# Performance work log

Measured on AMD Instinct MI355X. Metric: run time of the kernel, lower is better.

The kernel has to match this reference:

```python
import jax, jax.numpy as jnp
import numpy as np

B, C_IN, C_MID, C_OUT, H, W = 256, 2, 128, 64, 15, 15
N_RES = 4  # line_length//2 - 1 with line_length=11

# per-direction input offsets for kernel taps w0 and w2 (w1 is always center),
# matching fix_direction_order=True sparse 3x3 kernel construction:
# dir0 horizontal, dir1 vertical, dir2 anti-diagonal, dir3 main diagonal.
OFFSETS = (((0, -1), (0, 1)),
           ((-1, 0), (1, 0)),
           ((1, -1), (-1, 1)),
           ((-1, -1), (1, 1)))


def shift2d(x, di, dj):
    # out[..., i, j] = x[..., i+di, j+dj] with zero padding (di,dj in {-1,0,1})
    nd = x.ndim
    xp = jnp.pad(x, [(0, 0)] * (nd - 2) + [(1, 1), (1, 1)])
    h, w = x.shape[-2], x.shape[-1]
    return xp[..., 1 + di:1 + di + h, 1 + dj:1 + dj + w]


def dir_conv(x, w, b):
    # x: [4,B,Cin,H,W]; w: [Cout,Cin,3]; b: [Cout]
    x0 = jnp.stack([shift2d(x[d], *OFFSETS[d][0]) for d in range(4)])
    x2 = jnp.stack([shift2d(x[d], *OFFSETS[d][1]) for d in range(4)])
    y = (jnp.einsum('oc,dbchw->dbohw', w[..., 0], x0)
         + jnp.einsum('oc,dbchw->dbohw', w[..., 1], x)
         + jnp.einsum('oc,dbchw->dbohw', w[..., 2], x2))
    return y + b[None, None, :, None, None]


def conv1x1(x, w, b):
    # x: [4,B,Cin,H,W]; w: [Cout,Cin]; b: [Cout]
    return jnp.einsum('oc,dbchw->dbohw', w, x) + b[None, None, :, None, None]


def setup_inputs() -> dict:
    key = jax.random.key(0)
    ks = jax.random.split(key, 16)
    s_in = 1.0 / np.sqrt(3 * C_IN)
    s_mid = 1.0 / np.sqrt(3 * C_MID)
    s_pw = 1.0 / np.sqrt(C_MID)
    return {
        'x': jax.random.normal(ks[0], (B, C_IN, H, W), jnp.float32),
        'dconv0_w': jax.random.normal(ks[1], (C_MID, C_IN, 3), jnp.float32) * s_in,
        'dconv0_b': jnp.zeros((C_MID,), jnp.float32),
        'res_dconv_w': jax.random.normal(ks[2], (N_RES, C_MID, C_MID, 3), jnp.float32) * s_mid,
        'res_dconv_b': jnp.zeros((N_RES, C_MID), jnp.float32),
        'res_pw_w': jax.random.normal(ks[3], (N_RES, C_MID, C_MID), jnp.float32) * s_pw,
        'res_pw_b': jnp.zeros((N_RES, C_MID), jnp.float32),
        'c0_w1': jax.random.normal(ks[4], (C_MID, C_MID), jnp.float32) * s_pw,
        'c0_b1': jnp.zeros((C_MID,), jnp.float32),
        'c0_w2': jax.random.normal(ks[5], (C_MID, C_MID), jnp.float32) * s_pw,
        'c0_b2': jnp.zeros((C_MID,), jnp.float32),
        'final_w': jax.random.normal(ks[6], (C_OUT, C_MID), jnp.float32) * s_pw,
        'final_b': jnp.zeros((C_OUT,), jnp.float32),
    }


def reference(x, dconv0_w, dconv0_b, res_dconv_w, res_dconv_b,
              res_pw_w, res_pw_b, c0_w1, c0_b1, c0_w2, c0_b2,
              final_w, final_b):
    act = jax.nn.silu
    # all 4 direction streams start from the same input plane
    h = jnp.broadcast_to(x[None], (4,) + x.shape)  # [4,B,Cin,H,W]
    h = act(dir_conv(h, dconv0_w, dconv0_b))
    # DirectionalConvResBlocks (norm='none')
    for i in range(N_RES):
        r = h
        h = act(dir_conv(h, res_dconv_w[i], res_dconv_b[i]))
        h = act(conv1x1(h, res_pw_w[i], res_pw_b[i]))
        h = h + r
    # Conv0dResBlock (two 1x1 convs, middle_dim_multipler=1)
    r = h
    h = act(conv1x1(h, c0_w1, c0_b1))
    h = act(conv1x1(h, c0_w2, c0_b2))
    h = h + r
    # final 1x1 conv, then stack directions at dim=1 -> [B,4,Cout,H,W]
    h = conv1x1(h, final_w, final_b)
    return jnp.transpose(h, (1, 0, 2, 3, 4))
```

## Files before the change

kernel.cpp:

```cpp
#include <hip/hip_runtime.h>

using u16 = unsigned short;
using u32 = unsigned int;

typedef __bf16 bf16x8 __attribute__((ext_vector_type(8)));
typedef float  f32x4  __attribute__((ext_vector_type(4)));

#define NPOS   225
#define NT     15
#define ROWP   136
#define A_ROWS 289
#define B_ROWS 241
#define A_ELEMS (A_ROWS*ROWP)
#define B_ELEMS (B_ROWS*ROWP)
#define LDS_BYTES ((A_ELEMS + B_ELEMS)*2)
#define RSTRIDE17 (17*ROWP)

#define WA_PER_L 49152
#define WP_OFF   (4*WA_PER_L)
#define WP_PER   16384
#define WF_OFF   (WP_OFF + 6*WP_PER)
#define W_U16_TOTAL (WF_OFF + 8192)

__device__ __forceinline__ float bflo(u32 q){ return __uint_as_float(q << 16); }
__device__ __forceinline__ float bfhi(u32 q){ return __uint_as_float(q & 0xffff0000u); }
__device__ __forceinline__ u16 f2bf(float f){
  u32 u = __float_as_uint(f);
  return (u16)((u + 0x7fffu + ((u >> 16) & 1u)) >> 16);
}
__device__ __forceinline__ u32 packbf(float a, float b){
  union { __bf16 h[2]; u32 u; } r;
  r.h[0] = (__bf16)a; r.h[1] = (__bf16)b;
  return r.u;
}
__device__ __forceinline__ float silu_f(float x){
  return x * __builtin_amdgcn_rcpf(1.f + __expf(-x));
}
__device__ __forceinline__ f32x4 mfma16(bf16x8 a, bf16x8 b, f32x4 c){
  return __builtin_amdgcn_mfma_f32_16x16x32_bf16(a, b, c, 0, 0, 0);
}

__global__ void prep_w(const float* __restrict__ d0w, const float* __restrict__ rdw,
                       const float* __restrict__ rpw, const float* __restrict__ c1w,
                       const float* __restrict__ c2w, const float* __restrict__ fw,
                       float* __restrict__ ws)
{
  u16* wsb = (u16*)(ws + 768);
  const int total = 768 + W_U16_TOTAL;
  for (int idx = blockIdx.x*blockDim.x + threadIdx.x; idx < total; idx += gridDim.x*blockDim.x){
    if (idx < 768){
      int k = idx >> 7, o = idx & 127;
      ws[idx] = d0w[o*6 + k];
      continue;
    }
    int e = idx - 768;
    float v;
    if (e < WP_OFF){
      int L = e / WA_PER_L, r = e % WA_PER_L;
      int w = r / 6144, r2 = r % 6144;
      int t = r2 >> 11, r3 = r2 & 2047;
      int kb = r3 >> 9, r4 = r3 & 511;
      int l = r4 >> 3, j = r4 & 7;
      int o = w*16 + (l & 15);
      int c = kb*32 + ((l >> 4) << 3) + j;
      v = rdw[((L*128 + o)*128 + c)*3 + t];
    } else if (e < WF_OFF){
      int t2 = e - WP_OFF;
      int i = t2 / WP_PER, r = t2 % WP_PER;
      int w = r >> 11, r2 = r & 2047;
      int kb = r2 >> 9, r3 = r2 & 511;
      int l = r3 >> 3, j = r3 & 7;
      int o = w*16 + (l & 15);
      int c = kb*32 + ((l >> 4) << 3) + j;
      v = (i < 4) ? rpw[(i*128 + o)*128 + c]
        : (i == 4) ? c1w[o*128 + c] : c2w[o*128 + c];
    } else {
      int e2 = e - WF_OFF;
      int ot = e2 >> 11, r = e2 & 2047;
      int kb = r >> 9, r2 = r & 511;
      int l = r2 >> 3, j = r2 & 7;
      int o = ot*16 + (l & 15);
      int c = kb*32 + ((l >> 4) << 3) + j;
      v = fw[o*128 + c];
    }
    wsb[e] = f2bf(v);
  }
}

__device__ __forceinline__ void dconv_mfma(const u16* __restrict__ As, u16* __restrict__ Bs,
    const u16* __restrict__ wloc, const float* __restrict__ bias,
    int lane, int og, int T0, int T1, int off0, int off2)
{
  const int col = lane & 15, kg = lane >> 4, koff = kg*8;
  bf16x8 wa[2][12];
  #pragma unroll
  for (int ot=0; ot<2; ++ot)
    #pragma unroll
    for (int f=0; f<12; ++f)
      wa[ot][f] = *(const bf16x8*)(wloc + (2*og+ot)*6144 + f*512 + lane*8);
  f32x4 bz0 = *(const f32x4*)(bias + (2*og)*16 + kg*4);
  f32x4 bz1 = *(const f32x4*)(bias + (2*og+1)*16 + kg*4);
  const int c1 = (col+1)*ROWP;
  #pragma unroll 1
  for (int tile=T0; tile<T1; ++tile){
    int rb = (tile+1)*RSTRIDE17 + c1;
    const u16* s0 = As + rb + off0 + koff;
    const u16* s1 = As + rb + koff;
    const u16* s2 = As + rb + off2 + koff;
    f32x4 a0 = bz0, a1 = bz1;
    #pragma unroll
    for (int kb=0; kb<4; ++kb){
      bf16x8 v0 = *(const bf16x8*)(s0 + kb*32);
      bf16x8 v1 = *(const bf16x8*)(s1 + kb*32);
      bf16x8 v2 = *(const bf16x8*)(s2 + kb*32);
      a0 = mfma16(wa[0][kb],   v0, a0); a1 = mfma16(wa[1][kb],   v0, a1);
      a0 = mfma16(wa[0][4+kb], v1, a0); a1 = mfma16(wa[1][4+kb], v1, a1);
      a0 = mfma16(wa[0][8+kb], v2, a0); a1 = mfma16(wa[1][8+kb], v2, a1);
    }
    if (col < 15){
      u16* dp = Bs + (tile*16+col)*ROWP + og*32 + kg*4;
      uint2 w0; w0.x = packbf(silu_f(a0[0]), silu_f(a0[1]));
      w0.y = packbf(silu_f(a0[2]), silu_f(a0[3]));
      *(uint2*)dp = w0;
      uint2 w1; w1.x = packbf(silu_f(a1[0]), silu_f(a1[1]));
      w1.y = packbf(silu_f(a1[2]), silu_f(a1[3]));
      *(uint2*)(dp+16) = w1;
    }
  }
}

template<bool SRC_HALO, bool DST_HALO, bool RESID>
__device__ __forceinline__ void pw_mfma(const u16* __restrict__ src, u16* __restrict__ dst,
    const u16* __restrict__ wloc, const float* __restrict__ bias,
    int lane, int og, int T0, int T1)
{
  const int col = lane & 15, kg = lane >> 4, koff = kg*8;
  bf16x8 wp[2][4];
  #pragma unroll
  for (int ot=0; ot<2; ++ot)
    #pragma unroll
    for (int kb=0; kb<4; ++kb)
      wp[ot][kb] = *(const bf16x8*)(wloc + (2*og+ot)*2048 + kb*512 + lane*8);
  f32x4 bz0 = *(const f32x4*)(bias + (2*og)*16 + kg*4);
  f32x4 bz1 = *(const f32x4*)(bias + (2*og+1)*16 + kg*4);
  const int c1 = (col+1)*ROWP;
  #pragma unroll 1
  for (int tile=T0; tile<T1; ++tile){
    int rsrc = SRC_HALO ? (tile+1)*RSTRIDE17 + c1 : (tile*16+col)*ROWP;
    int rdst = DST_HALO ? (tile+1)*RSTRIDE17 + c1 : (tile*16+col)*ROWP;
    const u16* s = src + rsrc + koff;
    f32x4 a0 = bz0, a1 = bz1;
    #pragma unroll
    for (int kb=0; kb<4; ++kb){
      bf16x8 v = *(const bf16x8*)(s + kb*32);
      a0 = mfma16(wp[0][kb], v, a0);
      a1 = mfma16(wp[1][kb], v, a1);
    }
    if (col < 15){
      u16* dp = dst + rdst + og*32 + kg*4;
      float s0 = silu_f(a0[0]), s1 = silu_f(a0[1]), s2 = silu_f(a0[2]), s3 = silu_f(a0[3]);
      float t0 = silu_f(a1[0]), t1 = silu_f(a1[1]), t2 = silu_f(a1[2]), t3 = silu_f(a1[3]);
      if (RESID){
        uint2 r0 = *(const uint2*)dp;
        uint2 r1 = *(const uint2*)(dp+16);
        s0 += bflo(r0.x); s1 += bfhi(r0.x); s2 += bflo(r0.y); s3 += bfhi(r0.y);
        t0 += bflo(r1.x); t1 += bfhi(r1.x); t2 += bflo(r1.y); t3 += bfhi(r1.y);
      }
      uint2 w0; w0.x = packbf(s0, s1); w0.y = packbf(s2, s3);
      *(uint2*)dp = w0;
      uint2 w1; w1.x = packbf(t0, t1); w1.y = packbf(t2, t3);
      *(uint2*)(dp+16) = w1;
    }
  }
}

__global__ void __launch_bounds__(512, 2)
mix9_main(const float* __restrict__ x,
          const float* __restrict__ b_d0,
          const float* __restrict__ b_rd,
          const float* __restrict__ b_rp,
          const float* __restrict__ b_c1,
          const float* __restrict__ b_c2,
          const float* __restrict__ b_fin,
          const float* __restrict__ wt,
          float* __restrict__ out)
{
  extern __shared__ u16 sm[];
  u16* As = sm;
  u16* Bs = sm + A_ELEMS;

  const int blk  = blockIdx.x;
  const int b    = blk >> 2, d = blk & 3;
  const int tid  = threadIdx.x;
  const int wave = __builtin_amdgcn_readfirstlane(tid >> 6);
  const int lane = tid & 63;
  const int og   = wave >> 1;
  const int ph   = wave & 1;
  const int T0   = ph * 8;
  const int T1   = ph ? NT : 8;
  const int ob   = wave * 16;

  const int DI0[4] = {0,-1, 1,-1}, DJ0[4] = {-1, 0,-1,-1};
  const int DI2[4] = {0, 1,-1, 1}, DJ2[4] = { 1, 0, 1, 1};
  const int di0 = DI0[d], dj0 = DJ0[d], di2 = DI2[d], dj2 = DJ2[d];
  const int off0 = (di0*17 + dj0)*ROWP;
  const int off2 = (di2*17 + dj2)*ROWP;

  for (int k2 = tid; k2 < A_ELEMS; k2 += 512) As[k2] = 0;
  float* xs = (float*)Bs;
  for (int k2 = tid; k2 < 2*NPOS; k2 += 512) xs[k2] = x[b*(2*NPOS) + k2];
  __syncthreads();

  #pragma unroll 1
  for (int pb = 0; pb < 4; ++pb){
    int pp = pb*64 + lane;
    int i = pp >> 4, j = pp & 15;
    if (i >= 15 || j >= 15) continue;
    float acc[16];
    #pragma unroll
    for (int oo=0;oo<16;++oo) acc[oo] = b_d0[ob+oo];
    #pragma unroll
    for (int c=0;c<2;++c){
      int i0=i+di0, j0=j+dj0, i2=i+di2, j2=j+dj2;
      float x0 = ((unsigned)i0<15u && (unsigned)j0<15u) ? xs[c*NPOS + i0*15 + j0] : 0.f;
      float x1 = xs[c*NPOS + i*15 + j];
      float x2 = ((unsigned)i2<15u && (unsigned)j2<15u) ? xs[c*NPOS + i2*15 + j2] : 0.f;
      const float* w0r = wt + (c*3+0)*128 + ob;
      const float* w1r = wt + (c*3+1)*128 + ob;
      const float* w2r = wt + (c*3+2)*128 + ob;
      #pragma unroll
      for (int oo=0;oo<16;++oo)
        acc[oo] = fmaf(w0r[oo],x0, fmaf(w1r[oo],x1, fmaf(w2r[oo],x2, acc[oo])));
    }
    u16* dp = As + ((i+1)*17 + (j+1))*ROWP + ob;
    #pragma unroll
    for (int oo=0;oo<16;oo+=2)
      *(u32*)(dp+oo) = packbf(silu_f(acc[oo]), silu_f(acc[oo+1]));
  }
  __syncthreads();

  const u16* wsb = (const u16*)(wt + 768);

  #pragma unroll 1
  for (int L = 0; L < 4; ++L){
    dconv_mfma(As, Bs, wsb + L*WA_PER_L, b_rd + L*128, lane, og, T0, T1, off0, off2);
    __syncthreads();
    pw_mfma<false,true,true>(Bs, As, wsb + WP_OFF + L*WP_PER, b_rp + L*128, lane, og, T0, T1);
    __syncthreads();
  }

  pw_mfma<true,false,false>(As, Bs, wsb + WP_OFF + 4*WP_PER, b_c1, lane, og, T0, T1);
  __syncthreads();
  pw_mfma<false,true,true>(Bs, As, wsb + WP_OFF + 5*WP_PER, b_c2, lane, og, T0, T1);
  __syncthreads();

  {
    const int col = lane & 15, kg = lane >> 4, koff = kg*8;
    const u16* wl = wsb + WF_OFF + og*2048;
    bf16x8 wf[4];
    #pragma unroll
    for (int kb=0;kb<4;++kb) wf[kb] = *(const bf16x8*)(wl + (kb*64 + lane)*8);
    f32x4 bias4 = *(const f32x4*)(b_fin + og*16 + kg*4);
    const int c1 = (col+1)*ROWP;
    #pragma unroll 1
    for (int tile = T0; tile < T1; ++tile){
      int rb = (tile+1)*RSTRIDE17 + c1;
      const u16* s = As + rb + koff;
      f32x4 acc = bias4;
      #pragma unroll
      for (int kb=0;kb<4;++kb)
        acc = mfma16(wf[kb], *(const bf16x8*)(s + kb*32), acc);
      if (col < 15){
        float* op = out + ((size_t)((b*4 + d)*64 + og*16 + kg*4))*NPOS + tile*15 + col;
        op[0]      = acc[0];
        op[NPOS]   = acc[1];
        op[2*NPOS] = acc[2];
        op[3*NPOS] = acc[3];
      }
    }
  }
}

extern "C" void kernel_launch(void* const* d_in, const int* in_sizes, int n_in,
                              void* d_out, int out_size, void* d_ws, size_t ws_size,
                              hipStream_t stream)
{
  const float* x     = (const float*)d_in[0];
  const float* w_d0  = (const float*)d_in[1];
  const float* b_d0  = (const float*)d_in[2];
  const float* w_rd  = (const float*)d_in[3];
  const float* b_rd  = (const float*)d_in[4];
  const float* w_rp  = (const float*)d_in[5];
  const float* b_rp  = (const float*)d_in[6];
  const float* w_c1  = (const float*)d_in[7];
  const float* b_c1  = (const float*)d_in[8];
  const float* w_c2  = (const float*)d_in[9];
  const float* b_c2  = (const float*)d_in[10];
  const float* w_fin = (const float*)d_in[11];
  const float* b_fin = (const float*)d_in[12];
  float* wt  = (float*)d_ws;
  float* out = (float*)d_out;

  prep_w<<<128, 512, 0, stream>>>(w_d0, w_rd, w_rp, w_c1, w_c2, w_fin, wt);

  (void)hipFuncSetAttribute((const void*)mix9_main,
                            hipFuncAttributeMaxDynamicSharedMemorySize, LDS_BYTES);
  mix9_main<<<1024, 512, LDS_BYTES, stream>>>(x, b_d0, b_rd, b_rp, b_c1, b_c2, b_fin, wt, out);
}
```

Baseline: 239.8 us.

## Swizzle LDS activation rows with XOR instead of padding; widen pointwise tiles

Replaces the padded 136-element LDS row stride with an unpadded 128-element stride and an XOR swizzle on the channel offset keyed by row index, intended to avoid bank conflicts while shrinking LDS footprint. The pointwise convs now assign 4 output tiles per wave over a quarter of the spatial tiles instead of 2 tiles over half, reusing each loaded activation vector across more MFMAs. It also adds s_setprio around MFMA blocks and unrolls the pointwise loop by 2. Risks include higher register pressure from 16 weight fragments and swizzle index math overhead.

New measurement: 257.3 us. 1.07x slower.

```diff
diff --git a/kernel.cpp b/kernel.cpp
--- a/kernel.cpp
+++ b/kernel.cpp
@@ -8,13 +8,11 @@
 
 #define NPOS   225
 #define NT     15
-#define ROWP   136
 #define A_ROWS 289
-#define B_ROWS 241
-#define A_ELEMS (A_ROWS*ROWP)
-#define B_ELEMS (B_ROWS*ROWP)
+#define B_ROWS 240
+#define A_ELEMS (A_ROWS*128)
+#define B_ELEMS (B_ROWS*128)
 #define LDS_BYTES ((A_ELEMS + B_ELEMS)*2)
-#define RSTRIDE17 (17*ROWP)
 
 #define WA_PER_L 49152
 #define WP_OFF   (4*WA_PER_L)
@@ -89,9 +87,10 @@
 
 __device__ __forceinline__ void dconv_mfma(const u16* __restrict__ As, u16* __restrict__ Bs,
     const u16* __restrict__ wloc, const float* __restrict__ bias,
-    int lane, int og, int T0, int T1, int off0, int off2)
-{
-  const int col = lane & 15, kg = lane >> 4, koff = kg*8;
+    int lane, int og, int T0, int T1, int dr0, int dr2)
+{
+  const int col = lane & 15, kg = lane >> 4;
+  const int k0 = kg*8;
   bf16x8 wa[2][12];
   #pragma unroll
   for (int ot=0; ot<2; ++ot)
@@ -100,77 +99,95 @@
       wa[ot][f] = *(const bf16x8*)(wloc + (2*og+ot)*6144 + f*512 + lane*8);
   f32x4 bz0 = *(const f32x4*)(bias + (2*og)*16 + kg*4);
   f32x4 bz1 = *(const f32x4*)(bias + (2*og+1)*16 + kg*4);
-  const int c1 = (col+1)*ROWP;
+  const int chb = og*32 + kg*4;
+  int r1 = (T0+1)*17 + col + 1;
+  int p2 = T0*16 + col;
   #pragma unroll 1
   for (int tile=T0; tile<T1; ++tile){
-    int rb = (tile+1)*RSTRIDE17 + c1;
-    const u16* s0 = As + rb + off0 + koff;
-    const u16* s1 = As + rb + koff;
-    const u16* s2 = As + rb + off2 + koff;
+    int ra = r1 + dr0, rc = r1 + dr2;
+    int sa = (ra&15)<<3, sb = (r1&15)<<3, sc = (rc&15)<<3;
+    const u16* A0 = As + (ra<<7);
+    const u16* A1 = As + (r1<<7);
+    const u16* A2 = As + (rc<<7);
     f32x4 a0 = bz0, a1 = bz1;
+    __builtin_amdgcn_s_setprio(1);
     #pragma unroll
     for (int kb=0; kb<4; ++kb){
-      bf16x8 v0 = *(const bf16x8*)(s0 + kb*32);
-      bf16x8 v1 = *(const bf16x8*)(s1 + kb*32);
-      bf16x8 v2 = *(const bf16x8*)(s2 + kb*32);
+      const int kk = k0 + kb*32;
+      bf16x8 v0 = *(const bf16x8*)(A0 + (kk ^ sa));
+      bf16x8 v1 = *(const bf16x8*)(A1 + (kk ^ sb));
+      bf16x8 v2 = *(const bf16x8*)(A2 + (kk ^ sc));
       a0 = mfma16(wa[0][kb],   v0, a0); a1 = mfma16(wa[1][kb],   v0, a1);
       a0 = mfma16(wa[0][4+kb], v1, a0); a1 = mfma16(wa[1][4+kb], v1, a1);
       a0 = mfma16(wa[0][8+kb], v2, a0); a1 = mfma16(wa[1][8+kb], v2, a1);
     }
+    __builtin_amdgcn_s_setprio(0);
     if (col < 15){
-      u16* dp = Bs + (tile*16+col)*ROWP + og*32 + kg*4;
+      int idx = (p2<<7) + (chb ^ ((p2&15)<<3));
       uint2 w0; w0.x = packbf(silu_f(a0[0]), silu_f(a0[1]));
       w0.y = packbf(silu_f(a0[2]), silu_f(a0[3]));
-      *(uint2*)dp = w0;
+      *(uint2*)(Bs + idx) = w0;
       uint2 w1; w1.x = packbf(silu_f(a1[0]), silu_f(a1[1]));
       w1.y = packbf(silu_f(a1[2]), silu_f(a1[3]));
-      *(uint2*)(dp+16) = w1;
-    }
+      *(uint2*)(Bs + (idx ^ 16)) = w1;
+    }
+    r1 += 17; p2 += 16;
   }
 }
 
 template<bool SRC_HALO, bool DST_HALO, bool RESID>
 __device__ __forceinline__ void pw_mfma(const u16* __restrict__ src, u16* __restrict__ dst,
     const u16* __restrict__ wloc, const float* __restrict__ bias,
-    int lane, int og, int T0, int T1)
-{
-  const int col = lane & 15, kg = lane >> 4, koff = kg*8;
-  bf16x8 wp[2][4];
+    int lane, int og2, int T0, int T1)
+{
+  const int col = lane & 15, kg = lane >> 4;
+  const int k0 = kg*8;
+  bf16x8 wp[4][4];
   #pragma unroll
-  for (int ot=0; ot<2; ++ot)
+  for (int ot=0; ot<4; ++ot)
     #pragma unroll
     for (int kb=0; kb<4; ++kb)
-      wp[ot][kb] = *(const bf16x8*)(wloc + (2*og+ot)*2048 + kb*512 + lane*8);
-  f32x4 bz0 = *(const f32x4*)(bias + (2*og)*16 + kg*4);
-  f32x4 bz1 = *(const f32x4*)(bias + (2*og+1)*16 + kg*4);
-  const int c1 = (col+1)*ROWP;
-  #pragma unroll 1
+      wp[ot][kb] = *(const bf16x8*)(wloc + (og2*4+ot)*2048 + kb*512 + lane*8);
+  f32x4 bz[4];
+  #pragma unroll
+  for (int ot=0; ot<4; ++ot) bz[ot] = *(const f32x4*)(bias + og2*64 + ot*16 + kg*4);
+  const int chb = og2*64 + kg*4;
+  int r1 = (T0+1)*17 + col + 1;
+  int p2 = T0*16 + col;
+  #pragma unroll 2
   for (int tile=T0; tile<T1; ++tile){
-    int rsrc = SRC_HALO ? (tile+1)*RSTRIDE17 + c1 : (tile*16+col)*ROWP;
-    int rdst = DST_HALO ? (tile+1)*RSTRIDE17 + c1 : (tile*16+col)*ROWP;
-    const u16* s = src + rsrc + koff;
-    f32x4 a0 = bz0, a1 = bz1;
+    int rs = SRC_HALO ? r1 : p2;
+    const u16* S = src + (rs<<7);
+    int ss = (rs&15)<<3;
+    f32x4 a0 = bz[0], a1 = bz[1], a2 = bz[2], a3 = bz[3];
+    __builtin_amdgcn_s_setprio(1);
     #pragma unroll
     for (int kb=0; kb<4; ++kb){
-      bf16x8 v = *(const bf16x8*)(s + kb*32);
+      bf16x8 v = *(const bf16x8*)(S + ((k0 + kb*32) ^ ss));
       a0 = mfma16(wp[0][kb], v, a0);
       a1 = mfma16(wp[1][kb], v, a1);
-    }
+      a2 = mfma16(wp[2][kb], v, a2);
+      a3 = mfma16(wp[3][kb], v, a3);
+    }
+    __builtin_amdgcn_s_setprio(0);
     if (col < 15){
-      u16* dp = dst + rdst + og*32 + kg*4;
-      float s0 = silu_f(a0[0]), s1 = silu_f(a0[1]), s2 = silu_f(a0[2]), s3 = silu_f(a0[3]);
-      float t0 = silu_f(a1[0]), t1 = silu_f(a1[1]), t2 = silu_f(a1[2]), t3 = silu_f(a1[3]);
-      if (RESID){
-        uint2 r0 = *(const uint2*)dp;
-        uint2 r1 = *(const uint2*)(dp+16);
-        s0 += bflo(r0.x); s1 += bfhi(r0.x); s2 += bflo(r0.y); s3 += bfhi(r0.y);
-        t0 += bflo(r1.x); t1 += bfhi(r1.x); t2 += bflo(r1.y); t3 += bfhi(r1.y);
+      int rd = DST_HALO ? r1 : p2;
+      int idx0 = (rd<<7) + (chb ^ ((rd&15)<<3));
+      f32x4 aa[4] = {a0, a1, a2, a3};
+      #pragma unroll
+      for (int ot=0; ot<4; ++ot){
+        int idx = idx0 ^ (ot<<4);
+        float s0 = silu_f(aa[ot][0]), s1 = silu_f(aa[ot][1]);
+        float s2 = silu_f(aa[ot][2]), s3 = silu_f(aa[ot][3]);
+        if (RESID){
+          uint2 r = *(const uint2*)(dst + idx);
+          s0 += bflo(r.x); s1 += bfhi(r.x); s2 += bflo(r.y); s3 += bfhi(r.y);
+        }
+        uint2 w0; w0.x = packbf(s0, s1); w0.y = packbf(s2, s3);
+        *(uint2*)(dst + idx) = w0;
       }
-      uint2 w0; w0.x = packbf(s0, s1); w0.y = packbf(s2, s3);
-      *(uint2*)dp = w0;
-      uint2 w1; w1.x = packbf(t0, t1); w1.y = packbf(t2, t3);
-      *(uint2*)(dp+16) = w1;
-    }
+    }
+    r1 += 17; p2 += 16;
   }
 }
 
@@ -198,13 +215,17 @@
   const int ph   = wave & 1;
   const int T0   = ph * 8;
   const int T1   = ph ? NT : 8;
+  const int og2  = wave >> 2;
+  const int ph4  = wave & 3;
+  const int T0p  = ph4 * 4;
+  const int T1p  = (ph4 == 3) ? NT : T0p + 4;
   const int ob   = wave * 16;
 
   const int DI0[4] = {0,-1, 1,-1}, DJ0[4] = {-1, 0,-1,-1};
   const int DI2[4] = {0, 1,-1, 1}, DJ2[4] = { 1, 0, 1, 1};
   const int di0 = DI0[d], dj0 = DJ0[d], di2 = DI2[d], dj2 = DJ2[d];
-  const int off0 = (di0*17 + dj0)*ROWP;
-  const int off2 = (di2*17 + dj2)*ROWP;
+  const int dr0 = di0*17 + dj0;
+  const int dr2 = di2*17 + dj2;
 
   for (int k2 = tid; k2 < A_ELEMS; k2 += 512) As[k2] = 0;
   float* xs = (float*)Bs;
@@ -232,10 +253,12 @@
       for (int oo=0;oo<16;++oo)
         acc[oo] = fmaf(w0r[oo],x0, fmaf(w1r[oo],x1, fmaf(w2r[oo],x2, acc[oo])));
     }
-    u16* dp = As + ((i+1)*17 + (j+1))*ROWP + ob;
+    int r = (i+1)*17 + (j+1);
+    int s = (r&15)<<3;
+    u16* rowp = As + (r<<7);
     #pragma unroll
     for (int oo=0;oo<16;oo+=2)
-      *(u32*)(dp+oo) = packbf(silu_f(acc[oo]), silu_f(acc[oo+1]));
+      *(u32*)(rowp + ((ob+oo) ^ s)) = packbf(silu_f(acc[oo]), silu_f(acc[oo+1]));
   }
   __syncthreads();
 
@@ -243,33 +266,34 @@
 
   #pragma unroll 1
   for (int L = 0; L < 4; ++L){
-    dconv_mfma(As, Bs, wsb + L*WA_PER_L, b_rd + L*128, lane, og, T0, T1, off0, off2);
+    dconv_mfma(As, Bs, wsb + L*WA_PER_L, b_rd + L*128, lane, og, T0, T1, dr0, dr2);
     __syncthreads();
-    pw_mfma<false,true,true>(Bs, As, wsb + WP_OFF + L*WP_PER, b_rp + L*128, lane, og, T0, T1);
+    pw_mfma<false,true,true>(Bs, As, wsb + WP_OFF + L*WP_PER, b_rp + L*128, lane, og2, T0p, T1p);
     __syncthreads();
   }
 
-  pw_mfma<true,false,false>(As, Bs, wsb + WP_OFF + 4*WP_PER, b_c1, lane, og, T0, T1);
+  pw_mfma<true,false,false>(As, Bs, wsb + WP_OFF + 4*WP_PER, b_c1, lane, og2, T0p, T1p);
   __syncthreads();
-  pw_mfma<false,true,true>(Bs, As, wsb + WP_OFF + 5*WP_PER, b_c2, lane, og, T0, T1);
+  pw_mfma<false,true,true>(Bs, As, wsb + WP_OFF + 5*WP_PER, b_c2, lane, og2, T0p, T1p);
   __syncthreads();
 
   {
-    const int col = lane & 15, kg = lane >> 4, koff = kg*8;
+    const int col = lane & 15, kg = lane >> 4;
+    const int k0 = kg*8;
     const u16* wl = wsb + WF_OFF + og*2048;
     bf16x8 wf[4];
     #pragma unroll
     for (int kb=0;kb<4;++kb) wf[kb] = *(const bf16x8*)(wl + (kb*64 + lane)*8);
     f32x4 bias4 = *(const f32x4*)(b_fin + og*16 + kg*4);
-    const int c1 = (col+1)*ROWP;
+    int r1 = (T0+1)*17 + col + 1;
     #pragma unroll 1
     for (int tile = T0; tile < T1; ++tile){
-      int rb = (tile+1)*RSTRIDE17 + c1;
-      const u16* s = As + rb + koff;
+      const u16* S = As + (r1<<7);
+      int ss = (r1&15)<<3;
       f32x4 acc = bias4;
       #pragma unroll
       for (int kb=0;kb<4;++kb)
-        acc = mfma16(wf[kb], *(const bf16x8*)(s + kb*32), acc);
+        acc = mfma16(wf[kb], *(const bf16x8*)(S + ((k0 + kb*32) ^ ss)), acc);
       if (col < 15){
         float* op = out + ((size_t)((b*4 + d)*64 + og*16 + kg*4))*NPOS + tile*15 + col;
         op[0]      = acc[0];
@@ -277,6 +301,7 @@
         op[2*NPOS] = acc[2];
         op[3*NPOS] = acc[3];
       }
+      r1 += 17;
     }
   }
 }
```

## Double block to 1024 threads and repartition waves across output tiles and channels

Applied to the files above, without the earlier changes.

The block grows from 8 to 16 waves. The directional conv gives each wave a single 16-channel output tile instead of two. The pointwise layers split the 15 position tiles four ways across wave groups, and the first layer and final conv are redistributed to match. s_setprio is raised around the MFMA loops and the pointwise tile loop is unrolled by 2. More waves per block can better hide LDS latency, but launch_bounds(1024,1) and the LDS size allow only one block per CU where two were allowed before, and each wave now reuses fewer A-fragment loads.

Result: no change. 244.3 us (+1.9%).

```diff
diff --git a/kernel.cpp b/kernel.cpp
--- a/kernel.cpp
+++ b/kernel.cpp
@@ -89,17 +89,14 @@
 
 __device__ __forceinline__ void dconv_mfma(const u16* __restrict__ As, u16* __restrict__ Bs,
     const u16* __restrict__ wloc, const float* __restrict__ bias,
-    int lane, int og, int T0, int T1, int off0, int off2)
+    int lane, int ot, int T0, int T1, int off0, int off2)
 {
   const int col = lane & 15, kg = lane >> 4, koff = kg*8;
-  bf16x8 wa[2][12];
+  bf16x8 wa[12];
   #pragma unroll
-  for (int ot=0; ot<2; ++ot)
-    #pragma unroll
-    for (int f=0; f<12; ++f)
-      wa[ot][f] = *(const bf16x8*)(wloc + (2*og+ot)*6144 + f*512 + lane*8);
-  f32x4 bz0 = *(const f32x4*)(bias + (2*og)*16 + kg*4);
-  f32x4 bz1 = *(const f32x4*)(bias + (2*og+1)*16 + kg*4);
+  for (int f=0; f<12; ++f)
+    wa[f] = *(const bf16x8*)(wloc + ot*6144 + f*512 + lane*8);
+  f32x4 bz = *(const f32x4*)(bias + ot*16 + kg*4);
   const int c1 = (col+1)*ROWP;
   #pragma unroll 1
   for (int tile=T0; tile<T1; ++tile){
@@ -107,24 +104,23 @@
     const u16* s0 = As + rb + off0 + koff;
     const u16* s1 = As + rb + koff;
     const u16* s2 = As + rb + off2 + koff;
-    f32x4 a0 = bz0, a1 = bz1;
+    f32x4 a0 = bz;
+    __builtin_amdgcn_s_setprio(1);
     #pragma unroll
     for (int kb=0; kb<4; ++kb){
       bf16x8 v0 = *(const bf16x8*)(s0 + kb*32);
       bf16x8 v1 = *(const bf16x8*)(s1 + kb*32);
       bf16x8 v2 = *(const bf16x8*)(s2 + kb*32);
-      a0 = mfma16(wa[0][kb],   v0, a0); a1 = mfma16(wa[1][kb],   v0, a1);
-      a0 = mfma16(wa[0][4+kb], v1, a0); a1 = mfma16(wa[1][4+kb], v1, a1);
-      a0 = mfma16(wa[0][8+kb], v2, a0); a1 = mfma16(wa[1][8+kb], v2, a1);
-    }
+      a0 = mfma16(wa[kb],   v0, a0);
+      a0 = mfma16(wa[4+kb], v1, a0);
+      a0 = mfma16(wa[8+kb], v2, a0);
+    }
+    __builtin_amdgcn_s_setprio(0);
     if (col < 15){
-      u16* dp = Bs + (tile*16+col)*ROWP + og*32 + kg*4;
+      u16* dp = Bs + (tile*16+col)*ROWP + ot*16 + kg*4;
       uint2 w0; w0.x = packbf(silu_f(a0[0]), silu_f(a0[1]));
       w0.y = packbf(silu_f(a0[2]), silu_f(a0[3]));
       *(uint2*)dp = w0;
-      uint2 w1; w1.x = packbf(silu_f(a1[0]), silu_f(a1[1]));
-      w1.y = packbf(silu_f(a1[2]), silu_f(a1[3]));
-      *(uint2*)(dp+16) = w1;
     }
   }
 }
@@ -132,7 +128,7 @@
 template<bool SRC_HALO, bool DST_HALO, bool RESID>
 __device__ __forceinline__ void pw_mfma(const u16* __restrict__ src, u16* __restrict__ dst,
     const u16* __restrict__ wloc, const float* __restrict__ bias,
-    int lane, int og, int T0, int T1)
+    int lane, int og2, int T0, int T1)
 {
   const int col = lane & 15, kg = lane >> 4, koff = kg*8;
   bf16x8 wp[2][4];
@@ -140,31 +136,36 @@
   for (int ot=0; ot<2; ++ot)
     #pragma unroll
     for (int kb=0; kb<4; ++kb)
-      wp[ot][kb] = *(const bf16x8*)(wloc + (2*og+ot)*2048 + kb*512 + lane*8);
-  f32x4 bz0 = *(const f32x4*)(bias + (2*og)*16 + kg*4);
-  f32x4 bz1 = *(const f32x4*)(bias + (2*og+1)*16 + kg*4);
+      wp[ot][kb] = *(const bf16x8*)(wloc + (og2*2+ot)*2048 + kb*512 + lane*8);
+  f32x4 bz0 = *(const f32x4*)(bias + og2*32 + kg*4);
+  f32x4 bz1 = *(const f32x4*)(bias + og2*32 + 16 + kg*4);
+  const int chb = og2*32 + kg*4;
   const int c1 = (col+1)*ROWP;
-  #pragma unroll 1
+  #pragma unroll 2
   for (int tile=T0; tile<T1; ++tile){
-    int rsrc = SRC_HALO ? (tile+1)*RSTRIDE17 + c1 : (tile*16+col)*ROWP;
-    int rdst = DST_HALO ? (tile+1)*RSTRIDE17 + c1 : (tile*16+col)*ROWP;
-    const u16* s = src + rsrc + koff;
+    int r1 = (tile+1)*17 + col + 1;
+    int p2 = tile*16 + col;
+    int rsrc = SRC_HALO ? r1*ROWP : p2*ROWP;
+    const u16* S = src + rsrc + koff;
     f32x4 a0 = bz0, a1 = bz1;
+    __builtin_amdgcn_s_setprio(1);
     #pragma unroll
     for (int kb=0; kb<4; ++kb){
-      bf16x8 v = *(const bf16x8*)(s + kb*32);
+      bf16x8 v = *(const bf16x8*)(S + kb*32);
       a0 = mfma16(wp[0][kb], v, a0);
       a1 = mfma16(wp[1][kb], v, a1);
     }
+    __builtin_amdgcn_s_setprio(0);
     if (col < 15){
-      u16* dp = dst + rdst + og*32 + kg*4;
+      int rdst = DST_HALO ? r1*ROWP : p2*ROWP;
+      u16* dp = dst + rdst + chb;
       float s0 = silu_f(a0[0]), s1 = silu_f(a0[1]), s2 = silu_f(a0[2]), s3 = silu_f(a0[3]);
       float t0 = silu_f(a1[0]), t1 = silu_f(a1[1]), t2 = silu_f(a1[2]), t3 = silu_f(a1[3]);
       if (RESID){
         uint2 r0 = *(const uint2*)dp;
-        uint2 r1 = *(const uint2*)(dp+16);
+        uint2 r1v = *(const uint2*)(dp+16);
         s0 += bflo(r0.x); s1 += bfhi(r0.x); s2 += bflo(r0.y); s3 += bfhi(r0.y);
-        t0 += bflo(r1.x); t1 += bfhi(r1.x); t2 += bflo(r1.y); t3 += bfhi(r1.y);
+        t0 += bflo(r1v.x); t1 += bfhi(r1v.x); t2 += bflo(r1v.y); t3 += bfhi(r1v.y);
       }
       uint2 w0; w0.x = packbf(s0, s1); w0.y = packbf(s2, s3);
       *(uint2*)dp = w0;
@@ -174,7 +175,7 @@
   }
 }
 
-__global__ void __launch_bounds__(512, 2)
+__global__ void __launch_bounds__(1024, 1)
 mix9_main(const float* __restrict__ x,
           const float* __restrict__ b_d0,
           const float* __restrict__ b_rd,
@@ -194,11 +195,17 @@
   const int tid  = threadIdx.x;
   const int wave = __builtin_amdgcn_readfirstlane(tid >> 6);
   const int lane = tid & 63;
-  const int og   = wave >> 1;
-  const int ph   = wave & 1;
-  const int T0   = ph * 8;
-  const int T1   = ph ? NT : 8;
-  const int ob   = wave * 16;
+
+  const int ogd  = wave >> 1;
+  const int phd  = wave & 1;
+  const int T0d  = phd * 8;
+  const int T1d  = phd ? NT : 8;
+  const int og2  = wave >> 2;
+  const int ph4  = wave & 3;
+  const int T0p  = ph4 * 4;
+  const int T1p  = (ph4 == 3) ? NT : T0p + 4;
+  const int ob   = (wave & 7) * 16;
+  const int phal = wave >> 3;
 
   const int DI0[4] = {0,-1, 1,-1}, DJ0[4] = {-1, 0,-1,-1};
   const int DI2[4] = {0, 1,-1, 1}, DJ2[4] = { 1, 0, 1, 1};
@@ -206,14 +213,14 @@
   const int off0 = (di0*17 + dj0)*ROWP;
   const int off2 = (di2*17 + dj2)*ROWP;
 
-  for (int k2 = tid; k2 < A_ELEMS; k2 += 512) As[k2] = 0;
+  for (int k2 = tid; k2 < A_ELEMS; k2 += 1024) As[k2] = 0;
   float* xs = (float*)Bs;
-  for (int k2 = tid; k2 < 2*NPOS; k2 += 512) xs[k2] = x[b*(2*NPOS) + k2];
+  for (int k2 = tid; k2 < 2*NPOS; k2 += 1024) xs[k2] = x[b*(2*NPOS) + k2];
   __syncthreads();
 
   #pragma unroll 1
-  for (int pb = 0; pb < 4; ++pb){
-    int pp = pb*64 + lane;
+  for (int pb = 0; pb < 2; ++pb){
+    int pp = phal*128 + pb*64 + lane;
     int i = pp >> 4, j = pp & 15;
     if (i >= 15 || j >= 15) continue;
     float acc[16];
@@ -243,35 +250,39 @@
 
   #pragma unroll 1
   for (int L = 0; L < 4; ++L){
-    dconv_mfma(As, Bs, wsb + L*WA_PER_L, b_rd + L*128, lane, og, T0, T1, off0, off2);
+    dconv_mfma(As, Bs, wsb + L*WA_PER_L, b_rd + L*128, lane, ogd, T0d, T1d, off0, off2);
     __syncthreads();
-    pw_mfma<false,true,true>(Bs, As, wsb + WP_OFF + L*WP_PER, b_rp + L*128, lane, og, T0, T1);
+    pw_mfma<false,true,true>(Bs, As, wsb + WP_OFF + L*WP_PER, b_rp + L*128, lane, og2, T0p, T1p);
     __syncthreads();
   }
 
-  pw_mfma<true,false,false>(As, Bs, wsb + WP_OFF + 4*WP_PER, b_c1, lane, og, T0, T1);
+  pw_mfma<true,false,false>(As, Bs, wsb + WP_OFF + 4*WP_PER, b_c1, lane, og2, T0p, T1p);
   __syncthreads();
-  pw_mfma<false,true,true>(Bs, As, wsb + WP_OFF + 5*WP_PER, b_c2, lane, og, T0, T1);
+  pw_mfma<false,true,true>(Bs, As, wsb + WP_OFF + 5*WP_PER, b_c2, lane, og2, T0p, T1p);
   __syncthreads();
 
   {
     const int col = lane & 15, kg = lane >> 4, koff = kg*8;
-    const u16* wl = wsb + WF_OFF + og*2048;
+    const int ogf = wave >> 2;
+    const int phf = wave & 3;
+    const int T0f = phf * 4;
+    const int T1f = (phf == 3) ? NT : T0f + 4;
+    const u16* wl = wsb + WF_OFF + ogf*2048;
     bf16x8 wf[4];
     #pragma unroll
     for (int kb=0;kb<4;++kb) wf[kb] = *(const bf16x8*)(wl + (kb*64 + lane)*8);
-    f32x4 bias4 = *(const f32x4*)(b_fin + og*16 + kg*4);
+    f32x4 bias4 = *(const f32x4*)(b_fin + ogf*16 + kg*4);
     const int c1 = (col+1)*ROWP;
     #pragma unroll 1
-    for (int tile = T0; tile < T1; ++tile){
+    for (int tile = T0f; tile < T1f; ++tile){
       int rb = (tile+1)*RSTRIDE17 + c1;
-      const u16* s = As + rb + koff;
+      const u16* S = As + rb + koff;
       f32x4 acc = bias4;
       #pragma unroll
       for (int kb=0;kb<4;++kb)
-        acc = mfma16(wf[kb], *(const bf16x8*)(s + kb*32), acc);
+        acc = mfma16(wf[kb], *(const bf16x8*)(S + kb*32), acc);
       if (col < 15){
-        float* op = out + ((size_t)((b*4 + d)*64 + og*16 + kg*4))*NPOS + tile*15 + col;
+        float* op = out + ((size_t)((b*4 + d)*64 + ogf*16 + kg*4))*NPOS + tile*15 + col;
         op[0]      = acc[0];
         op[NPOS]   = acc[1];
         op[2*NPOS] = acc[2];
@@ -305,5 +316,5 @@
 
   (void)hipFuncSetAttribute((const void*)mix9_main,
                             hipFuncAttributeMaxDynamicSharedMemorySize, LDS_BYTES);
-  mix9_main<<<1024, 512, LDS_BYTES, stream>>>(x, b_d0, b_rd, b_rp, b_c1, b_c2, b_fin, wt, out);
-}
+  mix9_main<<<1024, 1024, LDS_BYTES, stream>>>(x, b_d0, b_rd, b_rp, b_c1, b_c2, b_fin, wt, out);
+}
```

## Widen pointwise MFMA tiles to four output groups and add MFMA priority hints

Applied to the files above, without the earlier changes.

The pointwise and final 1x1 conv stages now split work as 2 output-channel halves by 4 tile quarters instead of 4 output groups by 2 tile halves. Each wave therefore reuses each loaded activation fragment across four (or two, in the final stage) MFMA output tiles, which cuts LDS reads per MFMA. The final conv also changes each wave's mapping from 16 output channels over half the tiles to 32 channels over a quarter of the tiles. s_setprio is raised around the MFMA loops to favour issuing matrix work. In exchange, weight fragments held in registers double in the pointwise stage, which adds register pressure at the 512x2 launch bounds and may cause spills.

Result: no change. 244.0 us (+1.7%).

```diff
diff --git a/kernel.cpp b/kernel.cpp
--- a/kernel.cpp
+++ b/kernel.cpp
@@ -98,8 +98,8 @@
     #pragma unroll
     for (int f=0; f<12; ++f)
       wa[ot][f] = *(const bf16x8*)(wloc + (2*og+ot)*6144 + f*512 + lane*8);
-  f32x4 bz0 = *(const f32x4*)(bias + (2*og)*16 + kg*4);
-  f32x4 bz1 = *(const f32x4*)(bias + (2*og+1)*16 + kg*4);
+  f32x4 bz0 = *(const f32x4*)(bias + og*32 + kg*4);
+  f32x4 bz1 = *(const f32x4*)(bias + og*32 + 16 + kg*4);
   const int c1 = (col+1)*ROWP;
   #pragma unroll 1
   for (int tile=T0; tile<T1; ++tile){
@@ -108,6 +108,7 @@
     const u16* s1 = As + rb + koff;
     const u16* s2 = As + rb + off2 + koff;
     f32x4 a0 = bz0, a1 = bz1;
+    __builtin_amdgcn_s_setprio(1);
     #pragma unroll
     for (int kb=0; kb<4; ++kb){
       bf16x8 v0 = *(const bf16x8*)(s0 + kb*32);
@@ -117,6 +118,7 @@
       a0 = mfma16(wa[0][4+kb], v1, a0); a1 = mfma16(wa[1][4+kb], v1, a1);
       a0 = mfma16(wa[0][8+kb], v2, a0); a1 = mfma16(wa[1][8+kb], v2, a1);
     }
+    __builtin_amdgcn_s_setprio(0);
     if (col < 15){
       u16* dp = Bs + (tile*16+col)*ROWP + og*32 + kg*4;
       uint2 w0; w0.x = packbf(silu_f(a0[0]), silu_f(a0[1]));
@@ -132,44 +134,92 @@
 template<bool SRC_HALO, bool DST_HALO, bool RESID>
 __device__ __forceinline__ void pw_mfma(const u16* __restrict__ src, u16* __restrict__ dst,
     const u16* __restrict__ wloc, const float* __restrict__ bias,
-    int lane, int og, int T0, int T1)
+    int lane, int og2, int T0, int T1)
 {
   const int col = lane & 15, kg = lane >> 4, koff = kg*8;
-  bf16x8 wp[2][4];
+  bf16x8 wp[4][4];
+  #pragma unroll
+  for (int ot=0; ot<4; ++ot)
+    #pragma unroll
+    for (int kb=0; kb<4; ++kb)
+      wp[ot][kb] = *(const bf16x8*)(wloc + (og2*4+ot)*2048 + kb*512 + lane*8);
+  f32x4 bz[4];
+  #pragma unroll
+  for (int ot=0; ot<4; ++ot) bz[ot] = *(const f32x4*)(bias + og2*64 + ot*16 + kg*4);
+  const int chb = og2*64 + kg*4;
+  const int c1 = (col+1)*ROWP;
+  #pragma unroll 2
+  for (int tile=T0; tile<T1; ++tile){
+    const int rh = (tile+1)*RSTRIDE17 + c1;
+    const int rc = (tile*16+col)*ROWP;
+    const u16* S = src + (SRC_HALO ? rh : rc) + koff;
+    f32x4 a0 = bz[0], a1 = bz[1], a2 = bz[2], a3 = bz[3];
+    __builtin_amdgcn_s_setprio(1);
+    #pragma unroll
+    for (int kb=0; kb<4; ++kb){
+      bf16x8 v = *(const bf16x8*)(S + kb*32);
+      a0 = mfma16(wp[0][kb], v, a0);
+      a1 = mfma16(wp[1][kb], v, a1);
+      a2 = mfma16(wp[2][kb], v, a2);
+      a3 = mfma16(wp[3][kb], v, a3);
+    }
+    __builtin_amdgcn_s_setprio(0);
+    if (col < 15){
+      u16* dp = dst + (DST_HALO ? rh : rc) + chb;
+      f32x4 aa[4] = {a0, a1, a2, a3};
+      #pragma unroll
+      for (int ot=0; ot<4; ++ot){
+        u16* dq = dp + ot*16;
+        float s0 = silu_f(aa[ot][0]), s1 = silu_f(aa[ot][1]);
+        float s2 = silu_f(aa[ot][2]), s3 = silu_f(aa[ot][3]);
+        if (RESID){
+          uint2 r = *(const uint2*)dq;
+          s0 += bflo(r.x); s1 += bfhi(r.x); s2 += bflo(r.y); s3 += bfhi(r.y);
+        }
+        uint2 w0v; w0v.x = packbf(s0, s1); w0v.y = packbf(s2, s3);
+        *(uint2*)dq = w0v;
+      }
+    }
+  }
+}
+
+__device__ __forceinline__ void fin_mfma(const u16* __restrict__ As,
+    const u16* __restrict__ wloc, const float* __restrict__ bias,
+    float* __restrict__ out, int lane, int ogf, int T0, int T1, int bd)
+{
+  const int col = lane & 15, kg = lane >> 4, koff = kg*8;
+  bf16x8 wf[2][4];
   #pragma unroll
   for (int ot=0; ot<2; ++ot)
     #pragma unroll
     for (int kb=0; kb<4; ++kb)
-      wp[ot][kb] = *(const bf16x8*)(wloc + (2*og+ot)*2048 + kb*512 + lane*8);
-  f32x4 bz0 = *(const f32x4*)(bias + (2*og)*16 + kg*4);
-  f32x4 bz1 = *(const f32x4*)(bias + (2*og+1)*16 + kg*4);
+      wf[ot][kb] = *(const bf16x8*)(wloc + (ogf*2+ot)*2048 + kb*512 + lane*8);
+  f32x4 bz0 = *(const f32x4*)(bias + ogf*32 + kg*4);
+  f32x4 bz1 = *(const f32x4*)(bias + ogf*32 + 16 + kg*4);
   const int c1 = (col+1)*ROWP;
   #pragma unroll 1
   for (int tile=T0; tile<T1; ++tile){
-    int rsrc = SRC_HALO ? (tile+1)*RSTRIDE17 + c1 : (tile*16+col)*ROWP;
-    int rdst = DST_HALO ? (tile+1)*RSTRIDE17 + c1 : (tile*16+col)*ROWP;
-    const u16* s = src + rsrc + koff;
+    const u16* S = As + (tile+1)*RSTRIDE17 + c1 + koff;
     f32x4 a0 = bz0, a1 = bz1;
+    __builtin_amdgcn_s_setprio(1);
     #pragma unroll
     for (int kb=0; kb<4; ++kb){
-      bf16x8 v = *(const bf16x8*)(s + kb*32);
-      a0 = mfma16(wp[0][kb], v, a0);
-      a1 = mfma16(wp[1][kb], v, a1);
-    }
+      bf16x8 v = *(const bf16x8*)(S + kb*32);
+      a0 = mfma16(wf[0][kb], v, a0);
+      a1 = mfma16(wf[1][kb], v, a1);
+    }
+    __builtin_amdgcn_s_setprio(0);
     if (col < 15){
-      u16* dp = dst + rdst + og*32 + kg*4;
-      float s0 = silu_f(a0[0]), s1 = silu_f(a0[1]), s2 = silu_f(a0[2]), s3 = silu_f(a0[3]);
-      float t0 = silu_f(a1[0]), t1 = silu_f(a1[1]), t2 = silu_f(a1[2]), t3 = silu_f(a1[3]);
-      if (RESID){
-        uint2 r0 = *(const uint2*)dp;
-        uint2 r1 = *(const uint2*)(dp+16);
-        s0 += bflo(r0.x); s1 += bfhi(r0.x); s2 += bflo(r0.y); s3 += bfhi(r0.y);
-        t0 += bflo(r1.x); t1 += bfhi(r1.x); t2 += bflo(r1.y); t3 += bfhi(r1.y);
-      }
-      uint2 w0; w0.x = packbf(s0, s1); w0.y = packbf(s2, s3);
-      *(uint2*)dp = w0;
-      uint2 w1; w1.x = packbf(t0, t1); w1.y = packbf(t2, t3);
-      *(uint2*)(dp+16) = w1;
+      float* op = out + ((size_t)(bd*64 + ogf*32 + kg*4))*NPOS + tile*15 + col;
+      op[0]      = a0[0];
+      op[NPOS]   = a0[1];
+      op[2*NPOS] = a0[2];
+      op[3*NPOS] = a0[3];
+      float* oq = op + 16*NPOS;
+      oq[0]      = a1[0];
+      oq[NPOS]   = a1[1];
+      oq[2*NPOS] = a1[2];
+      oq[3*NPOS] = a1[3];
     }
   }
 }
@@ -194,10 +244,15 @@
   const int tid  = threadIdx.x;
   const int wave = __builtin_amdgcn_readfirstlane(tid >> 6);
   const int lane = tid & 63;
-  const int og   = wave >> 1;
-  const int ph   = wave & 1;
-  const int T0   = ph * 8;
-  const int T1   = ph ? NT : 8;
+
+  const int ogd  = wave >> 1;
+  const int phd  = wave & 1;
+  const int T0d  = phd * 8;
+  const int T1d  = phd ? NT : 8;
+  const int og2  = wave >> 2;
+  const int ph4  = wave & 3;
+  const int T0p  = ph4 * 4;
+  const int T1p  = (ph4 == 3) ? NT : T0p + 4;
   const int ob   = wave * 16;
 
   const int DI0[4] = {0,-1, 1,-1}, DJ0[4] = {-1, 0,-1,-1};
@@ -243,42 +298,18 @@
 
   #pragma unroll 1
   for (int L = 0; L < 4; ++L){
-    dconv_mfma(As, Bs, wsb + L*WA_PER_L, b_rd + L*128, lane, og, T0, T1, off0, off2);
+    dconv_mfma(As, Bs, wsb + L*WA_PER_L, b_rd + L*128, lane, ogd, T0d, T1d, off0, off2);
     __syncthreads();
-    pw_mfma<false,true,true>(Bs, As, wsb + WP_OFF + L*WP_PER, b_rp + L*128, lane, og, T0, T1);
+    pw_mfma<false,true,true>(Bs, As, wsb + WP_OFF + L*WP_PER, b_rp + L*128, lane, og2, T0p, T1p);
     __syncthreads();
   }
 
-  pw_mfma<true,false,false>(As, Bs, wsb + WP_OFF + 4*WP_PER, b_c1, lane, og, T0, T1);
+  pw_mfma<true,false,false>(As, Bs, wsb + WP_OFF + 4*WP_PER, b_c1, lane, og2, T0p, T1p);
   __syncthreads();
-  pw_mfma<false,true,true>(Bs, As, wsb + WP_OFF + 5*WP_PER, b_c2, lane, og, T0, T1);
+  pw_mfma<false,true,true>(Bs, As, wsb + WP_OFF + 5*WP_PER, b_c2, lane, og2, T0p, T1p);
   __syncthreads();
 
-  {
-    const int col = lane & 15, kg = lane >> 4, koff = kg*8;
-    const u16* wl = wsb + WF_OFF + og*2048;
-    bf16x8 wf[4];
-    #pragma unroll
-    for (int kb=0;kb<4;++kb) wf[kb] = *(const bf16x8*)(wl + (kb*64 + lane)*8);
-    f32x4 bias4 = *(const f32x4*)(b_fin + og*16 + kg*4);
-    const int c1 = (col+1)*ROWP;
-    #pragma unroll 1
-    for (int tile = T0; tile < T1; ++tile){
-      int rb = (tile+1)*RSTRIDE17 + c1;
-      const u16* s = As + rb + koff;
-      f32x4 acc = bias4;
-      #pragma unroll
-      for (int kb=0;kb<4;++kb)
-        acc = mfma16(wf[kb], *(const bf16x8*)(s + kb*32), acc);
-      if (col < 15){
-        float* op = out + ((size_t)((b*4 + d)*64 + og*16 + kg*4))*NPOS + tile*15 + col;
-        op[0]      = acc[0];
-        op[NPOS]   = acc[1];
-        op[2*NPOS] = acc[2];
-        op[3*NPOS] = acc[3];
-      }
-    }
-  }
+  fin_mfma(As, wsb + WF_OFF, b_fin, out, lane, og2, T0p, T1p, b*4 + d);
 }
 
 extern "C" void kernel_launch(void* const* d_in, const int* in_sizes, int n_in,
```
